# Kernel tuning notes

Measured on AMD Instinct MI355X. Metric: run time of the kernel, lower is better.

The kernel has to match this reference:

```python
import jax, jax.numpy as jnp
import numpy as np

K = 32  # neighbors, from init kwarg k


def setup_inputs() -> dict:
    key = jax.random.key(0)
    k1, k2, k3, k4 = jax.random.split(key, 4)
    N_train, N_test, D = 32768, 4096, 64
    x_train = jax.random.normal(k1, (N_train, D), dtype=jnp.float32)
    y_train = jax.random.randint(k2, (N_train,), 0, 1000, dtype=jnp.int64)
    x_test = jax.random.normal(k3, (N_test, D), dtype=jnp.float32)
    w_train = jax.random.uniform(k4, (N_train,), dtype=jnp.float32)
    return {"x_train": x_train, "y_train": y_train, "x_test": x_test, "w_train": w_train}


def _cdist(a, b):
    # Euclidean distance matrix [Na, Nb], matching torch.cdist(p=2)
    a2 = jnp.sum(a * a, axis=-1, keepdims=True)          # [Na,1]
    b2 = jnp.sum(b * b, axis=-1)[None, :]                # [1,Nb]
    sq = a2 + b2 - 2.0 * (a @ b.T)
    return jnp.sqrt(jnp.maximum(sq, 0.0))


def reference(x_train, y_train, x_test, w_train):
    n_test = x_test.shape[0]
    n_train = x_train.shape[0]
    dists = _cdist(x_test, x_train)                      # [N_test, N_train]
    # k smallest distances -> negate and take top_k
    _, indices = jax.lax.top_k(-dists, K)                # [N_test, K]
    knn_labels = y_train[indices]                        # [N_test, K]
    knn_w = w_train[indices]                             # [N_test, K]
    # weighted scatter vote: vote_pool[j, y_train[i]] += w_train[i]
    rows = jnp.arange(n_test)[:, None]                   # [N_test, 1]
    vote_pool = jnp.zeros((n_test, n_train), dtype=jnp.float32)
    vote_pool = vote_pool.at[rows, knn_labels].add(knn_w)
    return jnp.argmax(vote_pool, axis=1)
```

## Files before the change

### kernel.cpp

```cpp
#include <hip/hip_runtime.h>

#define NTRAIN 32768
#define NTEST  4096
#define DIM    64
#define KSEL   32
#define NLAB   1000
#define NCH    16
#define CHCOLS 2048
#define SLOT   112
#define NBIN   256
#define SSAMP  8192
#define SRANK2 32
#define POOLCAP 1792
#define WCOEF  0.01f

using short8 = __attribute__((ext_vector_type(8))) short;
using f32x4  = __attribute__((ext_vector_type(4))) float;
typedef unsigned short u16;

__device__ __forceinline__ unsigned f2u(float f){
  unsigned b = __float_as_uint(f);
  return (b & 0x80000000u) ? ~b : (b | 0x80000000u);
}
__device__ __forceinline__ u16 f2b(float x){
  unsigned u = __float_as_uint(x);
  return (u16)((u + 0x7fffu + ((u >> 16) & 1u)) >> 16);
}

struct Sel {
  unsigned hist[2048];
  unsigned wsum[4];
  unsigned sB, sLess, sU;
  int sNeed;
};

__device__ unsigned radix_select(const unsigned* __restrict__ keys, int n,
                                 unsigned rank, Sel* s, int t, int* needOut)
{
  const int lane = t & 63, wid = t >> 6;
  unsigned target = rank, pref = 0;
  for (int lev = 0; lev < 3; ++lev){
    const int nb    = (lev == 2) ? 1024 : 2048;
    const int shift = (lev == 0) ? 21 : (lev == 1 ? 10 : 0);
    for (int q = t; q < nb; q += 256) s->hist[q] = 0;
    __syncthreads();
    for (int i = t; i < n; i += 256){
      unsigned u = keys[i];
      bool ok = (lev == 0) ? true
              : (lev == 1) ? ((u >> 21) == pref)
                           : ((u >> 10) == pref);
      if (ok) atomicAdd(&s->hist[(u >> shift) & (unsigned)(nb - 1)], 1u);
    }
    __syncthreads();
    const int g = nb / 256;
    unsigned sl = 0;
#pragma unroll
    for (int k = 0; k < 8; ++k) if (k < g) sl += s->hist[t*g + k];
    unsigned x = sl;
#pragma unroll
    for (int ofs = 1; ofs < 64; ofs <<= 1){
      unsigned v = __shfl_up(x, (unsigned)ofs, 64);
      if (lane >= ofs) x += v;
    }
    if (lane == 63) s->wsum[wid] = x;
    __syncthreads();
    unsigned woff = 0;
#pragma unroll
    for (int w = 0; w < 4; ++w) if (w < wid) woff += s->wsum[w];
    unsigned incl = x + woff;
    unsigned excl = incl - sl;
    if (excl < target && target <= incl){
      unsigned cum = excl; int b = t*g;
      while (cum + s->hist[b] < target){ cum += s->hist[b]; ++b; }
      s->sB = (unsigned)b; s->sLess = cum;
    }
    __syncthreads();
    unsigned B = s->sB, cl = s->sLess;
    target -= cl;
    if      (lev == 0) pref = B;
    else if (lev == 1) pref = (pref << 11) | B;
    else if (t == 0){ s->sU = (pref << 10) | B; s->sNeed = (int)target; }
  }
  __syncthreads();
  *needOut = s->sNeed;
  return s->sU;
}

__device__ void select32(const unsigned* ku, const unsigned* ki, int n,
                         Sel* s, unsigned* tieI, unsigned* selI,
                         int* selCnt, int* tieCnt, int t)
{
  int need;
  unsigned ustar = radix_select(ku, n, KSEL, s, t, &need);
  if (t == 0){ *selCnt = 0; *tieCnt = 0; }
  __syncthreads();
  for (int i = t; i < n; i += 256){
    unsigned u = ku[i];
    if (u < ustar){ int p = atomicAdd(selCnt, 1); if (p < 40) selI[p] = ki[i]; }
    else if (u == ustar){ int p = atomicAdd(tieCnt, 1); if (p < 256) tieI[p] = ki[i]; }
  }
  __syncthreads();
  int nT = *tieCnt; if (nT > 256) nT = 256;
  if (t < nT){
    unsigned my = tieI[t]; int r = 0;
    for (int k = 0; k < nT; ++k) r += (tieI[k] < my) ? 1 : 0;
    if (r < need){ int p = atomicAdd(selCnt, 1); if (p < 40) selI[p] = my; }
  }
  __syncthreads();
}

__global__ void calib(int* __restrict__ MT, int* __restrict__ JT,
                      int* __restrict__ okf)
{
  const int l = threadIdx.x;
  const int v = l & 15;
  short8 av, onev, kv;
  u16 vb  = f2b((float)(v + 1));
  u16 one = (u16)0x3F80;
#pragma unroll
  for (int e = 0; e < 8; ++e){
    ((u16*)&av)[e]   = vb;
    ((u16*)&onev)[e] = one;
    ((u16*)&kv)[e]   = f2b((float)((l >> 4)*8 + e + 1));
  }
  f32x4 dA = {0,0,0,0}, dB = {0,0,0,0}, dK = {0,0,0,0};
  dA = __builtin_amdgcn_mfma_f32_16x16x32_bf16(av, onev, dA, 0,0,0);
  dB = __builtin_amdgcn_mfma_f32_16x16x32_bf16(onev, av, dB, 0,0,0);
  dK = __builtin_amdgcn_mfma_f32_16x16x32_bf16(kv, kv, dK, 0,0,0);
  bool ok = true;
#pragma unroll
  for (int e = 0; e < 4; ++e){
    int mi = (int)(dA[e]*(1.0f/32.0f) + 0.5f) - 1;
    int ji = (int)(dB[e]*(1.0f/32.0f) + 0.5f) - 1;
    if (mi < 0 || mi > 15 || dA[e] != 32.0f*(float)(mi+1)) ok = false;
    if (ji < 0 || ji > 15 || dB[e] != 32.0f*(float)(ji+1)) ok = false;
    if (dK[e] != 11440.0f) ok = false;
    MT[l*4 + e] = mi & 15;
    JT[l*4 + e] = ji & 15;
  }
  unsigned long long bal = __ballot(ok);
  if (l == 0) okf[0] = (bal == ~0ull) ? 1 : 0;
}

__global__ __launch_bounds__(256) void prep(const float* __restrict__ xtr,
        u16* __restrict__ xtr16, float* __restrict__ hb2,
        float* __restrict__ stats)
{
  int j = blockIdx.x*256 + threadIdx.x;
  const float4* rp = (const float4*)(xtr + (size_t)j*DIM);
  u16* orow = xtr16 + (size_t)j*DIM;
  float s = 0.f;
#pragma unroll
  for (int q = 0; q < 16; ++q){
    float4 w = rp[q];
    uint2 pk;
    pk.x = (unsigned)f2b(w.x) | ((unsigned)f2b(w.y) << 16);
    pk.y = (unsigned)f2b(w.z) | ((unsigned)f2b(w.w) << 16);
    *(uint2*)(orow + q*4) = pk;
    s = fmaf(w.x,w.x,s); s = fmaf(w.y,w.y,s);
    s = fmaf(w.z,w.z,s); s = fmaf(w.w,w.w,s);
  }
  float hs = 0.5f * s;
  hb2[j] = hs;
  float r0 = hs, r1 = hs*hs, r2 = s;
#pragma unroll
  for (int msk = 1; msk < 64; msk <<= 1){
    r0 += __shfl_xor(r0, msk, 64);
    r1 += __shfl_xor(r1, msk, 64);
    r2 = fmaxf(r2, __shfl_xor(r2, msk, 64));
  }
  if ((threadIdx.x & 63) == 0){
    atomicAdd(&stats[0], r0);
    atomicAdd(&stats[1], r1);
    atomicMax((unsigned*)&stats[2], __float_as_uint(r2));
  }
}

__global__ __launch_bounds__(256) void prepT(const float* __restrict__ xtst,
        u16* __restrict__ xtst16, const float* __restrict__ stats,
        float* __restrict__ loT, float* __restrict__ bsT, float* __restrict__ Wt)
{
  int m = blockIdx.x*256 + threadIdx.x;
  const float4* rp = (const float4*)(xtst + (size_t)m*DIM);
  u16* orow = xtst16 + (size_t)m*DIM;
  float s = 0.f;
#pragma unroll
  for (int q = 0; q < 16; ++q){
    float4 w = rp[q];
    uint2 pk;
    pk.x = (unsigned)f2b(w.x) | ((unsigned)f2b(w.y) << 16);
    pk.y = (unsigned)f2b(w.z) | ((unsigned)f2b(w.w) << 16);
    *(uint2*)(orow + q*4) = pk;
    s = fmaf(w.x,w.x,s); s = fmaf(w.y,w.y,s);
    s = fmaf(w.z,w.z,s); s = fmaf(w.w,w.w,s);
  }
  const float invN = 1.0f/(float)NTRAIN;
  float C   = stats[0]*invN;
  float var = fmaxf(stats[1]*invN - C*C, 0.f);
  float mb  = __uint_as_float(*(const unsigned*)&stats[2]);
  float sig = sqrtf(var + s) + 1e-6f;
  loT[m] = C - 12.f*sig;
  bsT[m] = 16.f/sig;
  Wt[m]  = WCOEF * sqrtf(s * mb);
}

__global__ __launch_bounds__(256) void sampleT(const u16* __restrict__ xtr16,
        const u16* __restrict__ xtst16, const float* __restrict__ hb2,
        const float* __restrict__ loT, const float* __restrict__ bsT,
        const float* __restrict__ Wt, const int* __restrict__ MT,
        const int* __restrict__ JT, const int* __restrict__ okf,
        float* __restrict__ TfB, float* __restrict__ thrFB)
{
  __shared__ unsigned histL[16*NBIN];
  __shared__ float hbS[SSAMP];

  const int t = threadIdx.x, lane = t & 63, w = t >> 6;
  const int m0 = blockIdx.x * 16;
  if (okf[0] == 0){
    if (t < 16){ TfB[m0+t] = 0.f; thrFB[m0+t] = -3.0e38f; }
    return;
  }
  const int oprow = lane & 15, kgrp = lane >> 4;

  for (int i = t; i < 16*NBIN; i += 256) histL[i] = 0;
  for (int i = t; i < SSAMP; i += 256) hbS[i] = hb2[i];

  int Ml[4], Jl[4];
#pragma unroll
  for (int e = 0; e < 4; ++e){ Ml[e] = MT[lane*4+e]; Jl[e] = JT[lane*4+e]; }

  const u16* ap = xtst16 + (size_t)(m0 + oprow)*DIM + kgrp*8;
  short8 a00 = *(const short8*)ap;
  short8 a01 = *(const short8*)(ap + 32);

  float lo0[4], bs0[4];
#pragma unroll
  for (int e = 0; e < 4; ++e){
    lo0[e] = loT[m0 + Ml[e]]; bs0[e] = bsT[m0 + Ml[e]];
  }
  __syncthreads();

  const int wcol = w*(SSAMP/4);
  const u16* bp = xtr16 + (size_t)(wcol + oprow)*DIM + kgrp*8;

#pragma unroll 2
  for (int jt = 0; jt < SSAMP/64; ++jt){
    short8 b0 = *(const short8*)bp;
    short8 b1 = *(const short8*)(bp + 32);
    f32x4 c0 = {0.f,0.f,0.f,0.f};
    c0 = __builtin_amdgcn_mfma_f32_16x16x32_bf16(a00, b0, c0, 0,0,0);
    c0 = __builtin_amdgcn_mfma_f32_16x16x32_bf16(a01, b1, c0, 0,0,0);
    const int jl = wcol + jt*16;
#pragma unroll
    for (int e = 0; e < 4; ++e){
      float h = hbS[jl + Jl[e]];
      float f = (h - c0[e] - lo0[e]) * bs0[e];
      if (f < 161.f){
        int b = (f < 0.f) ? 0 : (int)f;
        atomicAdd(&histL[Ml[e]*NBIN + b], 1u);
      }
    }
    bp += 16*DIM;
  }
  __syncthreads();
  if (t < 16){
    const unsigned* h = &histL[t*NBIN];
    unsigned cum = 0; int b = -1;
    for (int i = 0; i <= 160; ++i){
      cum += h[i];
      if (cum >= SRANK2){ b = i; break; }
    }
    int m = m0 + t;
    if (b < 0){ TfB[m] = 0.f; thrFB[m] = -3.0e38f; }
    else {
      float Te = loT[m] + (float)(b + 1) / bsT[m];
      float Wv = Wt[m];
      TfB[m]   = Te + 1.0f*Wv;
      thrFB[m] = Te + 2.0f*Wv;
    }
  }
}

__global__ __launch_bounds__(256) void knnA(const u16* __restrict__ xtr16,
        const u16* __restrict__ xtst16, const float* __restrict__ hb2,
        const float* __restrict__ thrFB, const int* __restrict__ MT,
        const int* __restrict__ JT, const int* __restrict__ okf,
        unsigned* __restrict__ cnt2, u16* __restrict__ cand)
{
  __shared__ float hbS[CHCOLS];
  __shared__ u16 lbuf[32][SLOT];
  __shared__ unsigned lcnt[32];

  const int t = threadIdx.x, lane = t & 63, w = t >> 6;
  const int jc = blockIdx.x & (NCH-1), mg = blockIdx.x >> 4;
  const int m0 = mg*32, col0 = jc*CHCOLS;

  if (okf[0] == 0){
    if (t < 32) cnt2[(size_t)jc*NTEST + m0 + t] = 0xFFFFFFFFu;
    return;
  }
  const int oprow = lane & 15, kgrp = lane >> 4;

  if (t < 32) lcnt[t] = 0;
  for (int i = t; i < CHCOLS; i += 256) hbS[i] = hb2[col0 + i];

  int Ml[4], Jl[4];
#pragma unroll
  for (int e = 0; e < 4; ++e){ Ml[e] = MT[lane*4+e]; Jl[e] = JT[lane*4+e]; }

  const u16* ap = xtst16 + (size_t)(m0 + oprow)*DIM + kgrp*8;
  short8 a00 = *(const short8*)ap;
  short8 a01 = *(const short8*)(ap + 32);
  short8 a10 = *(const short8*)(ap + 16*DIM);
  short8 a11 = *(const short8*)(ap + 16*DIM + 32);

  float th0[4], th1[4];
#pragma unroll
  for (int e = 0; e < 4; ++e){
    th0[e] = thrFB[m0 + Ml[e]];
    th1[e] = thrFB[m0 + 16 + Ml[e]];
  }
  float tm0 = fmaxf(fmaxf(th0[0],th0[1]), fmaxf(th0[2],th0[3]));
  float tm1 = fmaxf(fmaxf(th1[0],th1[1]), fmaxf(th1[2],th1[3]));

  __syncthreads();

  const int wcol = w*(CHCOLS/4);
  const u16* bp = xtr16 + (size_t)(col0 + wcol + oprow)*DIM + kgrp*8;

#pragma unroll 2
  for (int jt = 0; jt < CHCOLS/64; ++jt){
    short8 b0 = *(const short8*)bp;
    short8 b1 = *(const short8*)(bp + 32);
    f32x4 c0 = {0.f,0.f,0.f,0.f}, c1 = {0.f,0.f,0.f,0.f};
    c0 = __builtin_amdgcn_mfma_f32_16x16x32_bf16(a00, b0, c0, 0,0,0);
    c0 = __builtin_amdgcn_mfma_f32_16x16x32_bf16(a01, b1, c0, 0,0,0);
    c1 = __builtin_amdgcn_mfma_f32_16x16x32_bf16(a10, b0, c1, 0,0,0);
    c1 = __builtin_amdgcn_mfma_f32_16x16x32_bf16(a11, b1, c1, 0,0,0);
    const int jl = wcol + jt*16;
    float h[4];
#pragma unroll
    for (int e = 0; e < 4; ++e) h[e] = hbS[jl + Jl[e]];
    float g0 = fmaxf(fmaxf(c0[0]-h[0], c0[1]-h[1]), fmaxf(c0[2]-h[2], c0[3]-h[3]));
    if (g0 + tm0 > 0.f){
#pragma unroll
      for (int e = 0; e < 4; ++e) if (h[e] - c0[e] < th0[e]){
        unsigned p = atomicAdd(&lcnt[Ml[e]], 1u);
        if (p < SLOT) lbuf[Ml[e]][p] = (u16)(jl + Jl[e]);
      }
    }
    float g1 = fmaxf(fmaxf(c1[0]-h[0], c1[1]-h[1]), fmaxf(c1[2]-h[2], c1[3]-h[3]));
    if (g1 + tm1 > 0.f){
#pragma unroll
      for (int e = 0; e < 4; ++e) if (h[e] - c1[e] < th1[e]){
        unsigned p = atomicAdd(&lcnt[16 + Ml[e]], 1u);
        if (p < SLOT) lbuf[16 + Ml[e]][p] = (u16)(jl + Jl[e]);
      }
    }
    bp += 16*DIM;
  }
  __syncthreads();
  if (t < 32) cnt2[(size_t)jc*NTEST + m0 + t] = lcnt[t];
  const unsigned* lb32 = (const unsigned*)lbuf;
  unsigned* c32 = (unsigned*)cand;
  for (int i = t; i < 32*(SLOT/2); i += 256){
    int ms = i / (SLOT/2), e = i - ms*(SLOT/2);
    c32[((size_t)(m0 + ms)*NCH + jc)*(SLOT/2) + e] = lb32[i];
  }
}

__global__ __launch_bounds__(256) void knnB(const float* __restrict__ x_train,
        const float* __restrict__ hb2, const float* __restrict__ x_test,
        const int* __restrict__ y_train, const float* __restrict__ w_train,
        const float* __restrict__ TfB, const int* __restrict__ okf,
        const unsigned* __restrict__ cnt2, const u16* __restrict__ cand,
        int* __restrict__ out)
{
  __shared__ unsigned ku[POOLCAP], ki[POOLCAP];
  __shared__ unsigned chunkKeys[1024];
  __shared__ Sel ss;
  __shared__ unsigned tieI[256];
  __shared__ unsigned selI[40];
  __shared__ unsigned selR[KSEL];
  __shared__ int selCnt, tieCnt, poolCnt, nBelow, badJ;
  __shared__ float votes[NLAB];
  __shared__ unsigned cntS[NCH];
  __shared__ int yv[KSEL]; __shared__ float wv[KSEL];

  const int t = threadIdx.x, m = blockIdx.x;
  float* aS = (float*)chunkKeys;
  if (t < DIM) aS[t] = x_test[(size_t)m*DIM + t];
  if (t < NCH) cntS[t] = cnt2[(size_t)t*NTEST + m];
  if (t == 0){ nBelow = 0; badJ = 0; }
  __syncthreads();

  bool ovf = (okf[0] == 0);
  unsigned offs[NCH+1]; offs[0] = 0;
#pragma unroll
  for (int jcc = 0; jcc < NCH; ++jcc){
    unsigned cc = cntS[jcc];
    if (cc > SLOT) ovf = true;
    offs[jcc+1] = offs[jcc] + ((cc > SLOT) ? SLOT : cc);
  }
  int c = (int)offs[NCH];
  bool mainok = !ovf && c >= KSEL;

  if (mainok){
#pragma unroll
    for (int jcc = 0; jcc < NCH; ++jcc){
      unsigned cc = cntS[jcc];
      for (unsigned i = t; i < cc; i += 256){
        unsigned v = cand[((size_t)m*NCH + jcc)*SLOT + i];
        if (v >= CHCOLS){ badJ = 1; v = 0; }
        ki[offs[jcc] + i] = (unsigned)(jcc*CHCOLS) + v;
      }
    }
    __syncthreads();
    if (badJ) mainok = false;
  }
  const float Tf = TfB[m];
  if (mainok){
    for (int i = t; i < c; i += 256){
      unsigned j = ki[i];
      const float4* rp = (const float4*)(x_train + (size_t)j*DIM);
      float s = 0.f;
#pragma unroll
      for (int q = 0; q < 16; ++q){
        float4 v  = rp[q];
        float4 av = *(const float4*)&aS[q*4];
        s = fmaf(av.x,v.x,s); s = fmaf(av.y,v.y,s);
        s = fmaf(av.z,v.z,s); s = fmaf(av.w,v.w,s);
      }
      float kf = hb2[j] - s;
      ku[i] = f2u(kf);
      if (kf < Tf) atomicAdd(&nBelow, 1);
    }
    __syncthreads();
    mainok = (nBelow >= KSEL);
  }

  if (mainok){
    select32(ku, ki, c, &ss, tieI, selI, &selCnt, &tieCnt, t);
    if (t < KSEL) selR[t] = selI[t];
    __syncthreads();
  } else {
    const float4* ap4 = (const float4*)(x_test + (size_t)m*DIM);
    if (t == 0) poolCnt = 0;
    __syncthreads();
    for (int ch = 0; ch < NTRAIN/1024; ++ch){
      const int j0 = ch*1024;
      for (int q = 0; q < 4; ++q){
        int j = j0 + q*256 + t;
        const float4* rp = (const float4*)(x_train + (size_t)j*DIM);
        float s = 0.f;
#pragma unroll
        for (int qq = 0; qq < 16; ++qq){
          float4 v  = rp[qq];
          float4 av = ap4[qq];
          s = fmaf(av.x,v.x,s); s = fmaf(av.y,v.y,s);
          s = fmaf(av.z,v.z,s); s = fmaf(av.w,v.w,s);
        }
        chunkKeys[q*256 + t] = f2u(hb2[j] - s);
      }
      __syncthreads();
      int need;
      unsigned ustar = radix_select(chunkKeys, 1024, KSEL, &ss, t, &need);
      for (int q = 0; q < 4; ++q){
        unsigned u = chunkKeys[q*256 + t];
        if (u <= ustar){
          int p = atomicAdd(&poolCnt, 1);
          if (p < POOLCAP){ ku[p] = u; ki[p] = (unsigned)(j0 + q*256 + t); }
        }
      }
      __syncthreads();
    }
    int n = poolCnt; if (n > POOLCAP) n = POOLCAP;
    select32(ku, ki, n, &ss, tieI, selI, &selCnt, &tieCnt, t);
    if (t < KSEL) selR[t] = selI[t];
    __syncthreads();
  }

  for (int q = t; q < NLAB; q += 256) votes[q] = 0.f;
  if (t < KSEL){
    unsigned my = selR[t]; int r = 0;
#pragma unroll
    for (int k = 0; k < KSEL; ++k) r += (selR[k] < my) ? 1 : 0;
    yv[r] = y_train[my]; wv[r] = w_train[my];
  }
  __syncthreads();
  if (t == 0){
    for (int r = 0; r < KSEL; ++r) votes[yv[r]] += wv[r];
  }
  __syncthreads();

  float* rv = (float*)ss.hist;
  int*   rl = (int*)(ss.hist + 256);
  float bv = -1.f; int bl = 0;
  for (int l = t; l < NLAB; l += 256){
    float v = votes[l];
    if (v > bv){ bv = v; bl = l; }
  }
  rv[t] = bv; rl[t] = bl;
  __syncthreads();
  for (int sred = 128; sred > 0; sred >>= 1){
    if (t < sred){
      if (rv[t+sred] > rv[t] || (rv[t+sred] == rv[t] && rl[t+sred] < rl[t])){
        rv[t] = rv[t+sred]; rl[t] = rl[t+sred];
      }
    }
    __syncthreads();
  }
  if (t == 0) out[m] = rl[0];
}

__global__ __launch_bounds__(256) void knn_legacy(
    const float* __restrict__ x_train, const float* __restrict__ x_test,
    const int* __restrict__ y_train, const float* __restrict__ w_train,
    int* __restrict__ out)
{
  __shared__ unsigned keys[16384];
  __shared__ Sel ss;
  __shared__ unsigned candU[64];
  __shared__ unsigned candI[64];
  __shared__ unsigned tieI[256];
  __shared__ int nCand, nTie;
  __shared__ float rv[256]; __shared__ int rl[256];

  float* votes = (float*)ss.hist;
  const int t = threadIdx.x;
  const int m = blockIdx.x;

  float a[DIM];
  const float* am = x_test + (size_t)m * DIM;
#pragma unroll
  for (int d = 0; d < DIM; ++d) a[d] = am[d];

  if (t == 0) nCand = 0;

  for (int h = 0; h < 2; ++h){
    __syncthreads();
    for (int i = 0; i < 64; ++i){
      int j = h*16384 + i*256 + t;
      const float4* bp = (const float4*)(x_train + (size_t)j * DIM);
      float s = 0.f;
#pragma unroll
      for (int q = 0; q < 16; ++q){
        float4 v = bp[q];
        float e0 = a[4*q]   - v.x, e1 = a[4*q+1] - v.y;
        float e2 = a[4*q+2] - v.z, e3 = a[4*q+3] - v.w;
        s = fmaf(e0,e0,s); s = fmaf(e1,e1,s); s = fmaf(e2,e2,s); s = fmaf(e3,e3,s);
      }
      keys[i*256 + t] = f2u(s);
    }
    __syncthreads();

    int need;
    unsigned ustar = radix_select(keys, 16384, KSEL, &ss, t, &need);
    if (t == 0) nTie = 0;
    __syncthreads();

    for (int i = 0; i < 64; ++i){
      unsigned u   = keys[i*256 + t];
      unsigned idx = (unsigned)(h*16384 + i*256 + t);
      if (u < ustar){
        int p = atomicAdd(&nCand, 1);
        if (p < 64){ candU[p] = u; candI[p] = idx; }
      } else if (u == ustar){
        int p = atomicAdd(&nTie, 1);
        if (p < 256) tieI[p] = idx;
      }
    }
    __syncthreads();
    int nT = nTie; if (nT > 256) nT = 256;
    if (t < nT){
      unsigned my = tieI[t]; int r = 0;
      for (int k = 0; k < nT; ++k) r += (tieI[k] < my) ? 1 : 0;
      if (r < need){
        int p = atomicAdd(&nCand, 1);
        if (p < 64){ candU[p] = ustar; candI[p] = my; }
      }
    }
    __syncthreads();
  }

  for (int q = t; q < NLAB; q += 256) votes[q] = 0.f;
  __syncthreads();
  int nC = nCand; if (nC > 64) nC = 64;
  if (t < nC){
    unsigned mu = candU[t], mi = candI[t];
    int r = 0;
    for (int k = 0; k < nC; ++k){
      unsigned kku = candU[k], kki = candI[k];
      r += (kku < mu || (kku == mu && kki < mi)) ? 1 : 0;
    }
    if (r < KSEL){
      int lab = y_train[mi];
      atomicAdd(&votes[lab], w_train[mi]);
    }
  }
  __syncthreads();

  float bv = -1.f; int bl = 0;
  for (int l = t; l < NLAB; l += 256){
    float v = votes[l];
    if (v > bv){ bv = v; bl = l; }
  }
  rv[t] = bv; rl[t] = bl;
  __syncthreads();
  for (int s = 128; s > 0; s >>= 1){
    if (t < s){
      if (rv[t+s] > rv[t] || (rv[t+s] == rv[t] && rl[t+s] < rl[t])){
        rv[t] = rv[t+s]; rl[t] = rl[t+s];
      }
    }
    __syncthreads();
  }
  if (t == 0) out[m] = rl[0];
}

extern "C" void kernel_launch(void* const* d_in, const int* in_sizes, int n_in,
                              void* d_out, int out_size, void* d_ws, size_t ws_size,
                              hipStream_t stream)
{
  (void)in_sizes; (void)n_in; (void)out_size;
  const float* x_train = (const float*)d_in[0];
  const int*   y_train = (const int*)  d_in[1];
  const float* x_test  = (const float*)d_in[2];
  const float* w_train = (const float*)d_in[3];
  int* out = (int*)d_out;

  char* p = (char*)d_ws;
  u16*      xtr16  = (u16*)p;      p += (size_t)NTRAIN*DIM*2;
  u16*      xtst16 = (u16*)p;      p += (size_t)NTEST*DIM*2;
  float*    hb2    = (float*)p;    p += (size_t)NTRAIN*4;
  float*    loT    = (float*)p;    p += (size_t)NTEST*4;
  float*    bsT    = (float*)p;    p += (size_t)NTEST*4;
  float*    Wt     = (float*)p;    p += (size_t)NTEST*4;
  float*    TfB    = (float*)p;    p += (size_t)NTEST*4;
  float*    thrFB  = (float*)p;    p += (size_t)NTEST*4;
  unsigned* cnt2   = (unsigned*)p; p += (size_t)NCH*NTEST*4;
  int*      MT     = (int*)p;      p += 64*4*4;
  int*      JT     = (int*)p;      p += 64*4*4;
  int*      okf    = (int*)p;      p += 256;
  float*    stats  = (float*)p;    p += 512;
  u16*      cand   = (u16*)p;      p += (size_t)NTEST*NCH*SLOT*2;
  size_t need = (size_t)(p - (char*)d_ws);

  if (ws_size >= need){
    hipMemsetAsync(stats, 0, 512, stream);
    calib<<<1, 64, 0, stream>>>(MT, JT, okf);
    prep <<<NTRAIN/256, 256, 0, stream>>>(x_train, xtr16, hb2, stats);
    prepT<<<NTEST/256,  256, 0, stream>>>(x_test, xtst16, stats, loT, bsT, Wt);
    sampleT<<<NTEST/16, 256, 0, stream>>>(xtr16, xtst16, hb2, loT, bsT, Wt,
                                          MT, JT, okf, TfB, thrFB);
    knnA<<<(NTEST/32)*NCH, 256, 0, stream>>>(xtr16, xtst16, hb2, thrFB,
                                             MT, JT, okf, cnt2, cand);
    knnB<<<NTEST, 256, 0, stream>>>(x_train, hb2, x_test, y_train, w_train,
                                    TfB, okf, cnt2, cand, out);
  } else {
    knn_legacy<<<NTEST, 256, 0, stream>>>(x_train, x_test, y_train, w_train, out);
  }
}
```

Baseline: 307.8 us.

## Process four queries per block with one wavefront each in knnB

knnB now assigns one 64-lane wavefront per test query, four queries per block, and replaces the block-wide radix select with a wavefront-local rank sort over at most 512 candidates. Prefix sums, overflow checks and the argmax vote use wave shuffles and ballots instead of shared-memory atomics and block barriers. The fallback path becomes a wave-level streaming top-32 insertion over all training rows. The intent is to cut barrier and shared-memory overhead in the refine stage. The O(c^2) rank sort and the slow serial fallback could cost more when candidate counts are large or the fallback fires.

```diff
diff --git a/kernel.cpp b/kernel.cpp
--- a/kernel.cpp
+++ b/kernel.cpp
@@ -11,7 +11,7 @@
 #define NBIN   256
 #define SSAMP  8192
 #define SRANK2 32
-#define POOLCAP 1792
+#define SCAP2  512
 #define WCOEF  0.01f
 
 using short8 = __attribute__((ext_vector_type(8))) short;
@@ -84,29 +84,6 @@
   __syncthreads();
   *needOut = s->sNeed;
   return s->sU;
-}
-
-__device__ void select32(const unsigned* ku, const unsigned* ki, int n,
-                         Sel* s, unsigned* tieI, unsigned* selI,
-                         int* selCnt, int* tieCnt, int t)
-{
-  int need;
-  unsigned ustar = radix_select(ku, n, KSEL, s, t, &need);
-  if (t == 0){ *selCnt = 0; *tieCnt = 0; }
-  __syncthreads();
-  for (int i = t; i < n; i += 256){
-    unsigned u = ku[i];
-    if (u < ustar){ int p = atomicAdd(selCnt, 1); if (p < 40) selI[p] = ki[i]; }
-    else if (u == ustar){ int p = atomicAdd(tieCnt, 1); if (p < 256) tieI[p] = ki[i]; }
-  }
-  __syncthreads();
-  int nT = *tieCnt; if (nT > 256) nT = 256;
-  if (t < nT){
-    unsigned my = tieI[t]; int r = 0;
-    for (int k = 0; k < nT; ++k) r += (tieI[k] < my) ? 1 : 0;
-    if (r < need){ int p = atomicAdd(selCnt, 1); if (p < 40) selI[p] = my; }
-  }
-  __syncthreads();
 }
 
 __global__ void calib(int* __restrict__ MT, int* __restrict__ JT,
@@ -376,141 +353,163 @@
         const unsigned* __restrict__ cnt2, const u16* __restrict__ cand,
         int* __restrict__ out)
 {
-  __shared__ unsigned ku[POOLCAP], ki[POOLCAP];
-  __shared__ unsigned chunkKeys[1024];
-  __shared__ Sel ss;
-  __shared__ unsigned tieI[256];
-  __shared__ unsigned selI[40];
-  __shared__ unsigned selR[KSEL];
-  __shared__ int selCnt, tieCnt, poolCnt, nBelow, badJ;
-  __shared__ float votes[NLAB];
-  __shared__ unsigned cntS[NCH];
-  __shared__ int yv[KSEL]; __shared__ float wv[KSEL];
-
-  const int t = threadIdx.x, m = blockIdx.x;
-  float* aS = (float*)chunkKeys;
-  if (t < DIM) aS[t] = x_test[(size_t)m*DIM + t];
-  if (t < NCH) cntS[t] = cnt2[(size_t)t*NTEST + m];
-  if (t == 0){ nBelow = 0; badJ = 0; }
-  __syncthreads();
-
-  bool ovf = (okf[0] == 0);
-  unsigned offs[NCH+1]; offs[0] = 0;
-#pragma unroll
-  for (int jcc = 0; jcc < NCH; ++jcc){
-    unsigned cc = cntS[jcc];
-    if (cc > SLOT) ovf = true;
-    offs[jcc+1] = offs[jcc] + ((cc > SLOT) ? SLOT : cc);
-  }
-  int c = (int)offs[NCH];
-  bool mainok = !ovf && c >= KSEL;
-
+  __shared__ unsigned kiS[4][SCAP2];
+  __shared__ unsigned kuS[4][SCAP2];
+  __shared__ float    aS[4][DIM];
+  __shared__ unsigned selRS[4][KSEL];
+  __shared__ int      yvS[4][KSEL];
+  __shared__ float    wvS[4][KSEL];
+  __shared__ unsigned offsS[4][NCH+1];
+
+  const int t = threadIdx.x, lane = t & 63, w = t >> 6;
+  const int m = blockIdx.x*4 + w;
+
+  if (lane < DIM) aS[w][lane] = x_test[(size_t)m*DIM + lane];
+  unsigned cc = (lane < NCH) ? cnt2[(size_t)lane*NTEST + m] : 0u;
+  bool ovf = (okf[0] == 0) || (lane < NCH && cc > SLOT);
+  unsigned x = (lane < NCH) ? cc : 0u;
+#pragma unroll
+  for (int ofs = 1; ofs < NCH; ofs <<= 1){
+    unsigned v = __shfl_up(x, (unsigned)ofs, 64);
+    if (lane >= ofs) x += v;
+  }
+  if (lane < NCH) offsS[w][lane+1] = x;
+  if (lane == 0)  offsS[w][0] = 0;
+  bool anyovf = (__ballot(ovf) != 0ull);
+  const float Tf = TfB[m];
+  __syncthreads();
+
+  const int c = (int)offsS[w][NCH];
+  bool mainok = !anyovf && c >= KSEL && c <= SCAP2;
+
+  bool bad = false;
   if (mainok){
-#pragma unroll
-    for (int jcc = 0; jcc < NCH; ++jcc){
-      unsigned cc = cntS[jcc];
-      for (unsigned i = t; i < cc; i += 256){
-        unsigned v = cand[((size_t)m*NCH + jcc)*SLOT + i];
-        if (v >= CHCOLS){ badJ = 1; v = 0; }
-        ki[offs[jcc] + i] = (unsigned)(jcc*CHCOLS) + v;
-      }
-    }
-    __syncthreads();
-    if (badJ) mainok = false;
-  }
-  const float Tf = TfB[m];
+    for (int ch = 0; ch < NCH; ++ch){
+      unsigned base = offsS[w][ch];
+      unsigned n = offsS[w][ch+1] - base;
+      for (unsigned i = lane; i < n; i += 64){
+        unsigned v = cand[((size_t)m*NCH + ch)*SLOT + i];
+        bad |= (v >= CHCOLS);
+        kiS[w][base + i] = (unsigned)(ch*CHCOLS) + v;
+      }
+    }
+  }
+  if (__ballot(bad) != 0ull) mainok = false;
+  __syncthreads();
+
+  int nb = 0;
   if (mainok){
-    for (int i = t; i < c; i += 256){
-      unsigned j = ki[i];
+    for (int i = lane; i < c; i += 64){
+      unsigned j = kiS[w][i];
       const float4* rp = (const float4*)(x_train + (size_t)j*DIM);
       float s = 0.f;
 #pragma unroll
       for (int q = 0; q < 16; ++q){
         float4 v  = rp[q];
-        float4 av = *(const float4*)&aS[q*4];
+        float4 av = *(const float4*)&aS[w][q*4];
         s = fmaf(av.x,v.x,s); s = fmaf(av.y,v.y,s);
         s = fmaf(av.z,v.z,s); s = fmaf(av.w,v.w,s);
       }
       float kf = hb2[j] - s;
-      ku[i] = f2u(kf);
-      if (kf < Tf) atomicAdd(&nBelow, 1);
-    }
-    __syncthreads();
-    mainok = (nBelow >= KSEL);
-  }
+      kuS[w][i] = f2u(kf);
+      nb += (kf < Tf) ? 1 : 0;
+    }
+  }
+#pragma unroll
+  for (int ofs = 1; ofs < 64; ofs <<= 1) nb += __shfl_xor(nb, ofs, 64);
+  mainok = mainok && (nb >= KSEL);
+  __syncthreads();
 
   if (mainok){
-    select32(ku, ki, c, &ss, tieI, selI, &selCnt, &tieCnt, t);
-    if (t < KSEL) selR[t] = selI[t];
-    __syncthreads();
+    for (int i = lane; i < c; i += 64){
+      unsigned mu = kuS[w][i], mi = kiS[w][i];
+      int r = 0;
+      for (int k = 0; k < c; ++k){
+        unsigned kk = kuS[w][k], kj = kiS[w][k];
+        r += (kk < mu || (kk == mu && kj < mi)) ? 1 : 0;
+      }
+      if (r < KSEL) selRS[w][r] = mi;
+    }
   } else {
-    const float4* ap4 = (const float4*)(x_test + (size_t)m*DIM);
-    if (t == 0) poolCnt = 0;
-    __syncthreads();
-    for (int ch = 0; ch < NTRAIN/1024; ++ch){
-      const int j0 = ch*1024;
-      for (int q = 0; q < 4; ++q){
-        int j = j0 + q*256 + t;
-        const float4* rp = (const float4*)(x_train + (size_t)j*DIM);
-        float s = 0.f;
-#pragma unroll
-        for (int qq = 0; qq < 16; ++qq){
-          float4 v  = rp[qq];
-          float4 av = ap4[qq];
-          s = fmaf(av.x,v.x,s); s = fmaf(av.y,v.y,s);
-          s = fmaf(av.z,v.z,s); s = fmaf(av.w,v.w,s);
+    unsigned sk = 0xFFFFFFFFu, si = 0xFFFFFFFFu;
+    for (int batch = 0; batch < NTRAIN/64; ++batch){
+      int j = batch*64 + lane;
+      const float4* rp = (const float4*)(x_train + (size_t)j*DIM);
+      float s = 0.f;
+#pragma unroll
+      for (int q = 0; q < 16; ++q){
+        float4 v  = rp[q];
+        float4 av = *(const float4*)&aS[w][q*4];
+        s = fmaf(av.x,v.x,s); s = fmaf(av.y,v.y,s);
+        s = fmaf(av.z,v.z,s); s = fmaf(av.w,v.w,s);
+      }
+      unsigned ck = f2u(hb2[j] - s);
+      unsigned cj = (unsigned)j;
+      unsigned wk = sk, wi = si;
+#pragma unroll
+      for (int ofs = 1; ofs < 32; ofs <<= 1){
+        unsigned ok = __shfl_xor(wk, (unsigned)ofs, 32);
+        unsigned oi = __shfl_xor(wi, (unsigned)ofs, 32);
+        if (ok > wk || (ok == wk && oi > wi)){ wk = ok; wi = oi; }
+      }
+      unsigned wkb = __shfl(wk, 0, 64), wib = __shfl(wi, 0, 64);
+      bool q = (ck < wkb) || (ck == wkb && cj < wib);
+      unsigned long long mask = __ballot(q);
+      while (mask){
+        int sl = (int)__ffsll((unsigned long long)mask) - 1;
+        unsigned nk = __shfl(ck, sl, 64);
+        unsigned nj = __shfl(cj, sl, 64);
+        unsigned wk2 = sk, wi2 = si; int ws = lane & 31;
+#pragma unroll
+        for (int ofs = 1; ofs < 32; ofs <<= 1){
+          unsigned ok = __shfl_xor(wk2, (unsigned)ofs, 32);
+          unsigned oi = __shfl_xor(wi2, (unsigned)ofs, 32);
+          int      os = __shfl_xor(ws,  (unsigned)ofs, 32);
+          if (ok > wk2 || (ok == wk2 && oi > wi2)){ wk2 = ok; wi2 = oi; ws = os; }
         }
-        chunkKeys[q*256 + t] = f2u(hb2[j] - s);
-      }
-      __syncthreads();
-      int need;
-      unsigned ustar = radix_select(chunkKeys, 1024, KSEL, &ss, t, &need);
-      for (int q = 0; q < 4; ++q){
-        unsigned u = chunkKeys[q*256 + t];
-        if (u <= ustar){
-          int p = atomicAdd(&poolCnt, 1);
-          if (p < POOLCAP){ ku[p] = u; ki[p] = (unsigned)(j0 + q*256 + t); }
-        }
-      }
-      __syncthreads();
-    }
-    int n = poolCnt; if (n > POOLCAP) n = POOLCAP;
-    select32(ku, ki, n, &ss, tieI, selI, &selCnt, &tieCnt, t);
-    if (t < KSEL) selR[t] = selI[t];
-    __syncthreads();
-  }
-
-  for (int q = t; q < NLAB; q += 256) votes[q] = 0.f;
-  if (t < KSEL){
-    unsigned my = selR[t]; int r = 0;
-#pragma unroll
-    for (int k = 0; k < KSEL; ++k) r += (selR[k] < my) ? 1 : 0;
-    yv[r] = y_train[my]; wv[r] = w_train[my];
-  }
-  __syncthreads();
-  if (t == 0){
-    for (int r = 0; r < KSEL; ++r) votes[yv[r]] += wv[r];
-  }
-  __syncthreads();
-
-  float* rv = (float*)ss.hist;
-  int*   rl = (int*)(ss.hist + 256);
-  float bv = -1.f; int bl = 0;
-  for (int l = t; l < NLAB; l += 256){
-    float v = votes[l];
-    if (v > bv){ bv = v; bl = l; }
-  }
-  rv[t] = bv; rl[t] = bl;
-  __syncthreads();
-  for (int sred = 128; sred > 0; sred >>= 1){
-    if (t < sred){
-      if (rv[t+sred] > rv[t] || (rv[t+sred] == rv[t] && rl[t+sred] < rl[t])){
-        rv[t] = rv[t+sred]; rl[t] = rl[t+sred];
-      }
-    }
-    __syncthreads();
-  }
-  if (t == 0) out[m] = rl[0];
+        unsigned wk2b = __shfl(wk2, 0, 64), wi2b = __shfl(wi2, 0, 64);
+        int      wsb  = __shfl(ws, 0, 64);
+        bool ins = (nk < wk2b) || (nk == wk2b && nj < wi2b);
+        if (ins && lane == wsb){ sk = nk; si = nj; }
+        mask &= mask - 1;
+      }
+    }
+    int r = 0;
+#pragma unroll 8
+    for (int k = 0; k < 32; ++k){
+      unsigned ok = __shfl(sk, k, 64);
+      unsigned oi = __shfl(si, k, 64);
+      r += (ok < sk || (ok == sk && oi < si)) ? 1 : 0;
+    }
+    if (lane < 32) selRS[w][r] = si;
+  }
+  __syncthreads();
+
+  if (lane < KSEL){
+    unsigned my = selRS[w][lane];
+    int r2 = 0;
+#pragma unroll
+    for (int k = 0; k < KSEL; ++k) r2 += (selRS[w][k] < my) ? 1 : 0;
+    yvS[w][r2] = y_train[my];
+    wvS[w][r2] = w_train[my];
+  }
+  __syncthreads();
+
+  float ti = -1.0f; int li = 0x7fffffff;
+  if (lane < KSEL){
+    int myy = yvS[w][lane];
+    float s = 0.f;
+#pragma unroll
+    for (int k = 0; k < KSEL; ++k) if (yvS[w][k] == myy) s += wvS[w][k];
+    ti = s; li = myy;
+  }
+#pragma unroll
+  for (int ofs = 1; ofs < 64; ofs <<= 1){
+    float ov = __shfl_xor(ti, (unsigned)ofs, 64);
+    int   ol = __shfl_xor(li, (unsigned)ofs, 64);
+    if (ov > ti || (ov == ti && ol < li)){ ti = ov; li = ol; }
+  }
+  if (lane == 0) out[m] = li;
 }
 
 __global__ __launch_bounds__(256) void knn_legacy(
@@ -655,8 +654,8 @@
                                           MT, JT, okf, TfB, thrFB);
     knnA<<<(NTEST/32)*NCH, 256, 0, stream>>>(xtr16, xtst16, hb2, thrFB,
                                              MT, JT, okf, cnt2, cand);
-    knnB<<<NTEST, 256, 0, stream>>>(x_train, hb2, x_test, y_train, w_train,
-                                    TfB, okf, cnt2, cand, out);
+    knnB<<<NTEST/4, 256, 0, stream>>>(x_train, hb2, x_test, y_train, w_train,
+                                      TfB, okf, cnt2, cand, out);
   } else {
     knn_legacy<<<NTEST, 256, 0, stream>>>(x_train, x_test, y_train, w_train, out);
   }
```

Result: slower. 1.067 ms (median of 2 runs) (+246.5%).
